# Optimization experiments

Measured on AMD Instinct MI355X. Metric: run time of the kernel, lower is better.

## Reference

```python
import jax, jax.numpy as jnp
import numpy as np

DIM_HEAD = 64
HEADS = 8

def rotate_half(x):
    x1, x2 = jnp.split(x, 2, axis=-1)
    return jnp.concatenate((-x2, x1), axis=-1)

def apply_rope(pos, t):
    # pos: [N, d] broadcast against t: [B, H, N, d]
    return t * jnp.cos(pos) + rotate_half(t) * jnp.sin(pos)

def setup_inputs() -> dict:
    key = jax.random.key(0)
    k1, k2, k3, k4 = jax.random.split(key, 4)
    B, N, C = 2, 4096, 512
    inner = HEADS * DIM_HEAD
    x = jax.random.normal(k1, (B, N, C), dtype=jnp.float32)
    pos_emb = jax.random.normal(k2, (N, DIM_HEAD), dtype=jnp.float32)
    w_qkv = jax.random.normal(k3, (C, inner * 3), dtype=jnp.float32) * (1.0 / np.sqrt(C))
    w_out = jax.random.normal(k4, (inner, C), dtype=jnp.float32) * (1.0 / np.sqrt(inner))
    b_out = jnp.zeros((C,), dtype=jnp.float32)
    return {"x": x, "pos_emb": pos_emb, "w_qkv": w_qkv, "w_out": w_out, "b_out": b_out}

def reference(x, pos_emb, w_qkv, w_out, b_out):
    B, N, C = x.shape
    scale = DIM_HEAD ** -0.5
    qkv = x @ w_qkv  # [B, N, 3*inner]
    q, k, v = jnp.split(qkv, 3, axis=-1)
    def to_heads(t):
        return t.reshape(B, N, HEADS, DIM_HEAD).transpose(0, 2, 1, 3)  # [B,H,N,d]
    q, k, v = to_heads(q), to_heads(k), to_heads(v)
    q = apply_rope(pos_emb, q)
    k = apply_rope(pos_emb, k)
    dots = jnp.einsum('bhid,bhjd->bhij', q, k) * scale  # [B,H,N,N]
    attn = jax.nn.softmax(dots, axis=-1)
    out = jnp.einsum('bhij,bhjd->bhid', attn, v)
    out = out.transpose(0, 2, 1, 3).reshape(B, N, HEADS * DIM_HEAD)
    return out @ w_out + b_out
```

## Files before the change

### kernel.cpp

```cpp
#include <hip/hip_runtime.h>


typedef float    floatx4 __attribute__((ext_vector_type(4)));
typedef _Float16 half8   __attribute__((ext_vector_type(8)));
typedef _Float16 half4   __attribute__((ext_vector_type(4)));

__device__ __forceinline__ float fast_exp2(float x) {
#if __has_builtin(__builtin_amdgcn_exp2f)
  return __builtin_amdgcn_exp2f(x);
#else
  float r;
  asm("v_exp_f32 %0, %1" : "=v"(r) : "v"(x));
  return r;
#endif
}

__device__ __forceinline__ void async16(const void* g, void* l) {
  __builtin_amdgcn_global_load_lds(
      (const __attribute__((address_space(1))) void*)g,
      (__attribute__((address_space(3))) void*)l, 16, 0, 0);
}

__global__ __launch_bounds__(256) void prep(
    const float* __restrict__ X, const float* __restrict__ pos,
    const float* __restrict__ Wqkv, const float* __restrict__ Wout,
    _Float16* __restrict__ A2, float2* __restrict__ CSSN,
    _Float16* __restrict__ B2qkv, _Float16* __restrict__ B2out) {
  __shared__ float tile[64][65];
  const int bid = blockIdx.x, t = threadIdx.x;
  if (bid < 4096) {
    const int i = (bid * 256 + t) * 4;
    const float4 v = *(const float4*)(X + i);
    half4 h;
    h[0] = (_Float16)v.x; h[1] = (_Float16)v.y;
    h[2] = (_Float16)v.z; h[3] = (_Float16)v.w;
    *(half4*)(A2 + i) = h;
  } else if (bid < 5120) {
    const int i = (bid - 4096) * 256 + t;
    const float p = pos[i];
    CSSN[i] = make_float2(__cosf(p), __sinf(p));
  } else {
    const float* W; _Float16* B2T; int Ncols, bx, by;
    if (bid < 5312) { const int idx = bid - 5120; bx = idx % 24; by = idx / 24;
                      W = Wqkv; B2T = B2qkv; Ncols = 1536; }
    else            { const int idx = bid - 5312; bx = idx % 8;  by = idx / 8;
                      W = Wout; B2T = B2out; Ncols = 512; }
    const int k0 = by * 64, n0 = bx * 64;
    const int lane = t & 63, w = t >> 6;
#pragma unroll 4
    for (int i = 0; i < 16; ++i) {
      const int k = w * 16 + i;
      tile[k][lane] = W[(size_t)(k0 + k) * Ncols + n0 + lane];
    }
    __syncthreads();
#pragma unroll 4
    for (int i = 0; i < 16; ++i) {
      const int n = w * 16 + i;
      B2T[(size_t)(n0 + n) * 512 + k0 + lane] = (_Float16)tile[lane][n];
    }
  }
}

__global__ __launch_bounds__(256) void gemm_qkv_rope(
    const _Float16* __restrict__ A2, const _Float16* __restrict__ B2T,
    const float2* __restrict__ CSSN,
    _Float16* __restrict__ Qb, _Float16* __restrict__ Kb,
    _Float16* __restrict__ VT) {
  __shared__ __align__(16) _Float16 ldsA[128 * 64];
  __shared__ __align__(16) _Float16 ldsB[128 * 64];
  __shared__ __align__(16) _Float16 qk_lds[4][16][72];
  const int t = threadIdx.x, w = t >> 6, l = t & 63;
  const int lo = l & 15, hi = l >> 4, sw = lo & 7;
  const int m0 = blockIdx.y << 7, n0 = blockIdx.x << 7;

  const int strow = w * 8 + (l >> 3);
  const int schunk = (l & 7) ^ ((l >> 3) & 7);
  const _Float16* gA = A2 + (size_t)(m0 + strow) * 512 + schunk * 8;
  const _Float16* gB = B2T + (size_t)(n0 + strow) * 512 + schunk * 8;
  _Float16* lA = ldsA + w * 512 + l * 8;
  _Float16* lB = ldsB + w * 512 + l * 8;

  const int mw = (w >> 1) * 64, nw = (w & 1) * 64;

  floatx4 acc[4][4];
#pragma unroll
  for (int mt = 0; mt < 4; ++mt)
#pragma unroll
    for (int nt = 0; nt < 4; ++nt) acc[mt][nt] = (floatx4){0.f, 0.f, 0.f, 0.f};

  for (int ks = 0; ks < 8; ++ks) {
    const int kk = ks * 64;
    __syncthreads();
#pragma unroll
    for (int i = 0; i < 4; ++i) {
      async16(gA + (size_t)i * 32 * 512 + kk, lA + i * 2048);
      async16(gB + (size_t)i * 32 * 512 + kk, lB + i * 2048);
    }
    __syncthreads();
#pragma unroll
    for (int kc = 0; kc < 2; ++kc) {
      const int slot = ((hi + 4 * kc) ^ sw) * 8;
      half8 af[4], bf[4];
#pragma unroll
      for (int mt = 0; mt < 4; ++mt)
        af[mt] = *(const half8*)(ldsA + (mw + mt * 16 + lo) * 64 + slot);
#pragma unroll
      for (int nt = 0; nt < 4; ++nt)
        bf[nt] = *(const half8*)(ldsB + (nw + nt * 16 + lo) * 64 + slot);
#pragma unroll
      for (int mt = 0; mt < 4; ++mt)
#pragma unroll
        for (int nt = 0; nt < 4; ++nt)
          acc[mt][nt] = __builtin_amdgcn_mfma_f32_16x16x32_f16(
              af[mt], bf[nt], acc[mt][nt], 0, 0, 0);
    }
  }

  const int bx = blockIdx.x;
  const int kind = bx >> 2;
  const int h = ((bx & 3) << 1) | (nw >> 6);
  if (kind == 2) {
#pragma unroll
    for (int mt = 0; mt < 4; ++mt) {
      const int rowb = m0 + mw + mt * 16 + hi * 4;
      const int b = rowb >> 12, nn = rowb & 4095;
#pragma unroll
      for (int nt = 0; nt < 4; ++nt) {
        const int dd = nt * 16 + lo;
        half4 v4;
#pragma unroll
        for (int r = 0; r < 4; ++r) v4[r] = (_Float16)acc[mt][nt][r];
        *(half4*)(VT + ((size_t)((b * 8 + h) * 64 + dd)) * 4096 + nn) = v4;
      }
    }
  } else {
    _Float16* Db = (kind == 0) ? Qb : Kb;
    const float sc = (kind == 0) ? 0.125f * 1.44269504f : 1.0f;
    _Float16 (*qt_)[72] = qk_lds[w];
#pragma unroll
    for (int mt = 0; mt < 4; ++mt) {
#pragma unroll
      for (int r = 0; r < 4; ++r) {
        const int row = m0 + mw + mt * 16 + hi * 4 + r;
        const int nn = row & 4095;
        const float2* cp = CSSN + (size_t)nn * 64 + lo;
#pragma unroll
        for (int nt = 0; nt < 4; ++nt) {
          const float2 cs = cp[nt * 16];
          const float x0 = acc[mt][nt][r];
          const float xp = acc[mt][nt ^ 2][r];
          const float rot = (nt & 2) ? xp : -xp;
          qt_[hi * 4 + r][nt * 16 + lo] = (_Float16)((x0 * cs.x + rot * cs.y) * sc);
        }
      }
#pragma unroll
      for (int pass = 0; pass < 2; ++pass) {
        const int rr = pass * 8 + (l >> 3);
        const int dcol = (l & 7) * 8;
        const half8 v = *(const half8*)&qt_[rr][dcol];
        const int row = m0 + mw + mt * 16 + rr;
        const int b = row >> 12, nn = row & 4095;
        *(half8*)(Db + ((size_t)((b * 8 + h) * 4096 + nn)) * 64 + dcol) = v;
      }
    }
  }
}

__global__ __launch_bounds__(256) void gemm_out_f16(
    const _Float16* __restrict__ A2, const _Float16* __restrict__ B2T,
    const float* __restrict__ bias, float* __restrict__ C) {
  __shared__ __align__(16) _Float16 ldsA[128 * 64];
  __shared__ __align__(16) _Float16 ldsB[64 * 64];
  const int t = threadIdx.x, w = t >> 6, l = t & 63;
  const int lo = l & 15, hi = l >> 4, sw = lo & 7;
  const int m0 = blockIdx.y << 7, n0 = blockIdx.x << 6;

  const int strow = w * 8 + (l >> 3);
  const int schunk = (l & 7) ^ ((l >> 3) & 7);
  const _Float16* gA = A2 + (size_t)(m0 + strow) * 512 + schunk * 8;
  const _Float16* gB = B2T + (size_t)(n0 + strow) * 512 + schunk * 8;
  _Float16* lA = ldsA + w * 512 + l * 8;
  _Float16* lB = ldsB + w * 512 + l * 8;

  const int mw = (w >> 1) * 64, nw = (w & 1) * 32;

  floatx4 acc[4][2];
#pragma unroll
  for (int mt = 0; mt < 4; ++mt)
#pragma unroll
    for (int nt = 0; nt < 2; ++nt) acc[mt][nt] = (floatx4){0.f, 0.f, 0.f, 0.f};

  for (int ks = 0; ks < 8; ++ks) {
    const int kk = ks * 64;
    __syncthreads();
#pragma unroll
    for (int i = 0; i < 4; ++i)
      async16(gA + (size_t)i * 32 * 512 + kk, lA + i * 2048);
#pragma unroll
    for (int i = 0; i < 2; ++i)
      async16(gB + (size_t)i * 32 * 512 + kk, lB + i * 2048);
    __syncthreads();
#pragma unroll
    for (int kc = 0; kc < 2; ++kc) {
      const int slot = ((hi + 4 * kc) ^ sw) * 8;
      half8 af[4], bf[2];
#pragma unroll
      for (int mt = 0; mt < 4; ++mt)
        af[mt] = *(const half8*)(ldsA + (mw + mt * 16 + lo) * 64 + slot);
#pragma unroll
      for (int nt = 0; nt < 2; ++nt)
        bf[nt] = *(const half8*)(ldsB + (nw + nt * 16 + lo) * 64 + slot);
#pragma unroll
      for (int mt = 0; mt < 4; ++mt)
#pragma unroll
        for (int nt = 0; nt < 2; ++nt)
          acc[mt][nt] = __builtin_amdgcn_mfma_f32_16x16x32_f16(
              af[mt], bf[nt], acc[mt][nt], 0, 0, 0);
    }
  }
#pragma unroll
  for (int mt = 0; mt < 4; ++mt)
#pragma unroll
    for (int r = 0; r < 4; ++r) {
      const int row = m0 + mw + mt * 16 + hi * 4 + r;
#pragma unroll
      for (int nt = 0; nt < 2; ++nt) {
        const int col = n0 + nw + nt * 16 + lo;
        C[(size_t)row * 512 + col] = acc[mt][nt][r] + bias[col];
      }
    }
}

__global__ __launch_bounds__(256, 4) void flash_attn(
    const _Float16* __restrict__ Qb, const _Float16* __restrict__ Kb,
    const _Float16* __restrict__ VT, _Float16* __restrict__ Opart,
    float* __restrict__ lpart) {
  __shared__ __align__(16) _Float16 ldsK[64 * 64];
  __shared__ __align__(16) _Float16 ldsV[64 * 64];
  const int t = threadIdx.x;
  const int w = t >> 6, l = t & 63;
  const int lo = l & 15, hi = l >> 4;
  const int sw = lo & 7;
  const int bh = blockIdx.y, qt = blockIdx.x, sp = blockIdx.z;

  const int srow = l >> 3;
  const int scol = (l & 7) ^ srow;
  const int goffK = srow * 64 + scol * 8;
  const size_t goffV = (size_t)srow * 4096 + scol * 8;
  const int ldst = l * 8;

  const _Float16* Qrow = Qb + ((size_t)bh * 4096 + qt * 128 + w * 32 + lo) * 64;
  half8 qf[2][2];
  qf[0][0] = *(const half8*)(Qrow + hi * 8);
  qf[0][1] = *(const half8*)(Qrow + hi * 8 + 32);
  qf[1][0] = *(const half8*)(Qrow + 16 * 64 + hi * 8);
  qf[1][1] = *(const half8*)(Qrow + 16 * 64 + hi * 8 + 32);

  floatx4 acc[2][4];
  float l_s[2] = {0.f, 0.f};
#pragma unroll
  for (int g = 0; g < 2; ++g)
#pragma unroll
    for (int dt = 0; dt < 4; ++dt) acc[g][dt] = (floatx4){0.f, 0.f, 0.f, 0.f};

  const _Float16* Kt = Kb + (size_t)bh * 4096 * 64;
  const _Float16* Vt = VT + (size_t)bh * 64 * 4096;

  for (int tt = sp * 32; tt < sp * 32 + 32; ++tt) {
    __syncthreads();
    {
      const _Float16* gK = Kt + (size_t)tt * 4096;
      const _Float16* gV = Vt + tt * 64;
      const int k0 = w * 2;
      async16(gK + (size_t)k0 * 512 + goffK,       ldsK + k0 * 512 + ldst);
      async16(gK + (size_t)(k0 + 1) * 512 + goffK, ldsK + (k0 + 1) * 512 + ldst);
      async16(gV + (size_t)k0 * 32768 + goffV,       ldsV + k0 * 512 + ldst);
      async16(gV + (size_t)(k0 + 1) * 32768 + goffV, ldsV + (k0 + 1) * 512 + ldst);
    }
    __syncthreads();

    floatx4 st[2][4];
#pragma unroll
    for (int jt = 0; jt < 4; ++jt) {
      const _Float16* kr = ldsK + (jt * 16 + lo) * 64;
      const half8 kf0 = *(const half8*)(kr + ((hi ^ sw) * 8));
      const half8 kf1 = *(const half8*)(kr + (((hi + 4) ^ sw) * 8));
#pragma unroll
      for (int g = 0; g < 2; ++g) {
        floatx4 z = (floatx4){0.f, 0.f, 0.f, 0.f};
        z = __builtin_amdgcn_mfma_f32_16x16x32_f16(kf0, qf[g][0], z, 0, 0, 0);
        z = __builtin_amdgcn_mfma_f32_16x16x32_f16(kf1, qf[g][1], z, 0, 0, 0);
        st[g][jt] = z;
      }
    }

    half4 pf[2][4];
#pragma unroll
    for (int g = 0; g < 2; ++g)
#pragma unroll
      for (int jt = 0; jt < 4; ++jt) {
        const float e0 = fast_exp2(st[g][jt][0]);
        const float e1 = fast_exp2(st[g][jt][1]);
        const float e2 = fast_exp2(st[g][jt][2]);
        const float e3 = fast_exp2(st[g][jt][3]);
        l_s[g] += (e0 + e1) + (e2 + e3);
        uint2 u;
        u.x = __builtin_bit_cast(unsigned, __builtin_amdgcn_cvt_pkrtz(e0, e1));
        u.y = __builtin_bit_cast(unsigned, __builtin_amdgcn_cvt_pkrtz(e2, e3));
        pf[g][jt] = __builtin_bit_cast(half4, u);
      }

#pragma unroll
    for (int dt = 0; dt < 4; ++dt) {
      half4 vf[4];
#pragma unroll
      for (int jt = 0; jt < 4; ++jt)
        vf[jt] = *(const half4*)(ldsV + (dt * 16 + lo) * 64 +
                                 (((jt * 2 + (hi >> 1)) ^ sw) * 8) + (hi & 1) * 4);
#pragma unroll
      for (int g = 0; g < 2; ++g)
#pragma unroll
        for (int jt = 0; jt < 4; ++jt)
          acc[g][dt] = __builtin_amdgcn_mfma_f32_16x16x16f16(
              pf[g][jt], vf[jt], acc[g][dt], 0, 0, 0);
    }
  }

  _Float16* obase = Opart + ((size_t)(sp * 16 + bh)) * 4096 * 64;
  float*    lbase = lpart + ((size_t)(sp * 16 + bh)) * 4096;
#pragma unroll
  for (int g = 0; g < 2; ++g) {
    float v = l_s[g];
    v += __shfl_xor(v, 16);
    v += __shfl_xor(v, 32);
    if (hi == 0)
      lbase[qt * 128 + w * 32 + g * 16 + lo] = v;
#pragma unroll
    for (int r = 0; r < 4; ++r) {
      const int q = qt * 128 + w * 32 + g * 16 + hi * 4 + r;
#pragma unroll
      for (int dt = 0; dt < 4; ++dt)
        obase[(size_t)q * 64 + dt * 16 + lo] = (_Float16)acc[g][dt][r];
    }
  }
}

__global__ __launch_bounds__(256) void combine_splits(
    const _Float16* __restrict__ Opart, const float* __restrict__ lpart,
    _Float16* __restrict__ O2) {
  const int idx = blockIdx.x * 256 + threadIdx.x;
  const int d0 = (idx & 15) * 4;
  const int q  = (idx >> 4) & 4095;
  const int bh = idx >> 16;
  const int b = bh >> 3, h = bh & 7;
  const half4 a0 = *(const half4*)(Opart + ((size_t)bh * 4096 + q) * 64 + d0);
  const half4 a1 = *(const half4*)(Opart + ((size_t)(16 + bh) * 4096 + q) * 64 + d0);
  const float lsum = lpart[(size_t)bh * 4096 + q] +
                     lpart[(size_t)(16 + bh) * 4096 + q];
  const float inv = 1.f / lsum;
  half4 o;
#pragma unroll
  for (int i = 0; i < 4; ++i)
    o[i] = (_Float16)(((float)a0[i] + (float)a1[i]) * inv);
  *(half4*)(O2 + ((size_t)(b * 4096 + q)) * 512 + h * 64 + d0) = o;
}

extern "C" void kernel_launch(void* const* d_in, const int* in_sizes, int n_in,
                              void* d_out, int out_size, void* d_ws, size_t ws_size,
                              hipStream_t stream) {
  const float* x     = (const float*)d_in[0];
  const float* pos   = (const float*)d_in[1];
  const float* w_qkv = (const float*)d_in[2];
  const float* w_out = (const float*)d_in[3];
  const float* b_out = (const float*)d_in[4];
  float* out = (float*)d_out;

  char* ws = (char*)d_ws;
  if (ws_size < (size_t)56 * 1024 * 1024) return;

  const size_t MB = 1024 * 1024;
  _Float16* A2x   = (_Float16*)ws;
  _Float16* O2    = (_Float16*)ws;
  _Float16* B2qkv = (_Float16*)(ws + 8 * MB);
  float2*   CSSN  = (float2*)(ws + 11 * MB);
  _Float16* Qb    = (_Float16*)(ws + 13 * MB);
  _Float16* Kb    = (_Float16*)(ws + 21 * MB);
  _Float16* VT    = (_Float16*)(ws + 29 * MB);
  _Float16* Opart = (_Float16*)(ws + 37 * MB);
  float*    lpart = (float*)(ws + 53 * MB);
  _Float16* B2out = (_Float16*)(ws + 54 * MB);

  prep<<<5376, 256, 0, stream>>>(x, pos, w_qkv, w_out, A2x, CSSN, B2qkv, B2out);
  gemm_qkv_rope<<<dim3(12, 64), 256, 0, stream>>>(A2x, B2qkv, CSSN, Qb, Kb, VT);
  flash_attn<<<dim3(32, 16, 2), 256, 0, stream>>>(Qb, Kb, VT, Opart, lpart);
  combine_splits<<<4096, 256, 0, stream>>>(Opart, lpart, O2);
  gemm_out_f16<<<dim3(8, 64), 256, 0, stream>>>(O2, B2out, b_out, out);
}
```

Before: 206.3 us.

## Fuse split-combine into output GEMM and narrow QKV GEMM tiles

Drops the separate combine_splits kernel. The output projection GEMM now reads both flash-attention partial outputs and their row sums directly, normalizes them, and stores the result into LDS as its A operand, one head per K step. This saves a launch and a round trip of the combined O through global memory. The cost is that these A loads become synchronous register loads instead of async LDS loads. The QKV GEMM also changes from 128x128 to 128x64 tiles, doubling the grid and reusing ldsA as the RoPE staging buffer to cut LDS use, which lowers reuse per block.

```diff
diff --git a/kernel.cpp b/kernel.cpp
--- a/kernel.cpp
+++ b/kernel.cpp
@@ -67,11 +67,10 @@
     _Float16* __restrict__ Qb, _Float16* __restrict__ Kb,
     _Float16* __restrict__ VT) {
   __shared__ __align__(16) _Float16 ldsA[128 * 64];
-  __shared__ __align__(16) _Float16 ldsB[128 * 64];
-  __shared__ __align__(16) _Float16 qk_lds[4][16][72];
+  __shared__ __align__(16) _Float16 ldsB[64 * 64];
   const int t = threadIdx.x, w = t >> 6, l = t & 63;
   const int lo = l & 15, hi = l >> 4, sw = lo & 7;
-  const int m0 = blockIdx.y << 7, n0 = blockIdx.x << 7;
+  const int m0 = blockIdx.y << 7, n0 = blockIdx.x << 6;
 
   const int strow = w * 8 + (l >> 3);
   const int schunk = (l & 7) ^ ((l >> 3) & 7);
@@ -80,11 +79,11 @@
   _Float16* lA = ldsA + w * 512 + l * 8;
   _Float16* lB = ldsB + w * 512 + l * 8;
 
-  const int mw = (w >> 1) * 64, nw = (w & 1) * 64;
-
-  floatx4 acc[4][4];
-#pragma unroll
-  for (int mt = 0; mt < 4; ++mt)
+  const int mw = w * 32;
+
+  floatx4 acc[2][4];
+#pragma unroll
+  for (int mt = 0; mt < 2; ++mt)
 #pragma unroll
     for (int nt = 0; nt < 4; ++nt) acc[mt][nt] = (floatx4){0.f, 0.f, 0.f, 0.f};
 
@@ -92,23 +91,24 @@
     const int kk = ks * 64;
     __syncthreads();
 #pragma unroll
-    for (int i = 0; i < 4; ++i) {
+    for (int i = 0; i < 4; ++i)
       async16(gA + (size_t)i * 32 * 512 + kk, lA + i * 2048);
+#pragma unroll
+    for (int i = 0; i < 2; ++i)
       async16(gB + (size_t)i * 32 * 512 + kk, lB + i * 2048);
-    }
     __syncthreads();
 #pragma unroll
     for (int kc = 0; kc < 2; ++kc) {
       const int slot = ((hi + 4 * kc) ^ sw) * 8;
-      half8 af[4], bf[4];
-#pragma unroll
-      for (int mt = 0; mt < 4; ++mt)
+      half8 af[2], bf[4];
+#pragma unroll
+      for (int mt = 0; mt < 2; ++mt)
         af[mt] = *(const half8*)(ldsA + (mw + mt * 16 + lo) * 64 + slot);
 #pragma unroll
       for (int nt = 0; nt < 4; ++nt)
-        bf[nt] = *(const half8*)(ldsB + (nw + nt * 16 + lo) * 64 + slot);
-#pragma unroll
-      for (int mt = 0; mt < 4; ++mt)
+        bf[nt] = *(const half8*)(ldsB + (nt * 16 + lo) * 64 + slot);
+#pragma unroll
+      for (int mt = 0; mt < 2; ++mt)
 #pragma unroll
         for (int nt = 0; nt < 4; ++nt)
           acc[mt][nt] = __builtin_amdgcn_mfma_f32_16x16x32_f16(
@@ -117,11 +117,11 @@
   }
 
   const int bx = blockIdx.x;
-  const int kind = bx >> 2;
-  const int h = ((bx & 3) << 1) | (nw >> 6);
+  const int kind = bx >> 3;
+  const int h = bx & 7;
   if (kind == 2) {
 #pragma unroll
-    for (int mt = 0; mt < 4; ++mt) {
+    for (int mt = 0; mt < 2; ++mt) {
       const int rowb = m0 + mw + mt * 16 + hi * 4;
       const int b = rowb >> 12, nn = rowb & 4095;
 #pragma unroll
@@ -134,11 +134,12 @@
       }
     }
   } else {
-    _Float16* Db = (kind == 0) ? Qb : Kb;
+    _Float16* Db = kind ? Kb : Qb;
     const float sc = (kind == 0) ? 0.125f * 1.44269504f : 1.0f;
-    _Float16 (*qt_)[72] = qk_lds[w];
-#pragma unroll
-    for (int mt = 0; mt < 4; ++mt) {
+    __syncthreads();
+    _Float16 (*qt_)[72] = (_Float16(*)[72])(ldsA + w * 2048);
+#pragma unroll
+    for (int mt = 0; mt < 2; ++mt) {
 #pragma unroll
       for (int r = 0; r < 4; ++r) {
         const int row = m0 + mw + mt * 16 + hi * 4 + r;
@@ -167,17 +168,23 @@
 }
 
 __global__ __launch_bounds__(256) void gemm_out_f16(
-    const _Float16* __restrict__ A2, const _Float16* __restrict__ B2T,
-    const float* __restrict__ bias, float* __restrict__ C) {
+    const _Float16* __restrict__ Opart, const float* __restrict__ lpart,
+    const _Float16* __restrict__ B2T, const float* __restrict__ bias,
+    float* __restrict__ C) {
   __shared__ __align__(16) _Float16 ldsA[128 * 64];
   __shared__ __align__(16) _Float16 ldsB[64 * 64];
   const int t = threadIdx.x, w = t >> 6, l = t & 63;
   const int lo = l & 15, hi = l >> 4, sw = lo & 7;
   const int m0 = blockIdx.y << 7, n0 = blockIdx.x << 6;
+  const int b = m0 >> 12, q0 = m0 & 4095;
 
   const int strow = w * 8 + (l >> 3);
   const int schunk = (l & 7) ^ ((l >> 3) & 7);
-  const _Float16* gA = A2 + (size_t)(m0 + strow) * 512 + schunk * 8;
+  const size_t aRow = (size_t)(q0 + strow) * 64 + schunk * 8;
+  const _Float16* gA0 = Opart + ((size_t)(b * 8)) * 4096 * 64 + aRow;
+  const _Float16* gA1 = Opart + ((size_t)(16 + b * 8)) * 4096 * 64 + aRow;
+  const float* lp0 = lpart + (size_t)(b * 8) * 4096 + q0 + strow;
+  const float* lp1 = lpart + (size_t)(16 + b * 8) * 4096 + q0 + strow;
   const _Float16* gB = B2T + (size_t)(n0 + strow) * 512 + schunk * 8;
   _Float16* lA = ldsA + w * 512 + l * 8;
   _Float16* lB = ldsB + w * 512 + l * 8;
@@ -192,10 +199,20 @@
 
   for (int ks = 0; ks < 8; ++ks) {
     const int kk = ks * 64;
-    __syncthreads();
-#pragma unroll
-    for (int i = 0; i < 4; ++i)
-      async16(gA + (size_t)i * 32 * 512 + kk, lA + i * 2048);
+    const size_t hoff = (size_t)ks * 4096 * 64;
+    const int lhoff = ks * 4096;
+    __syncthreads();
+#pragma unroll
+    for (int i = 0; i < 4; ++i) {
+      const half8 o0 = *(const half8*)(gA0 + hoff + (size_t)i * 32 * 64);
+      const half8 o1 = *(const half8*)(gA1 + hoff + (size_t)i * 32 * 64);
+      const float ls = lp0[lhoff + i * 32] + lp1[lhoff + i * 32];
+      const _Float16 inv = (_Float16)(1.f / ls);
+      half8 s;
+#pragma unroll
+      for (int j = 0; j < 8; ++j) s[j] = (_Float16)((o0[j] + o1[j]) * inv);
+      *(half8*)(lA + i * 2048) = s;
+    }
 #pragma unroll
     for (int i = 0; i < 2; ++i)
       async16(gB + (size_t)i * 32 * 512 + kk, lB + i * 2048);
@@ -345,26 +362,6 @@
   }
 }
 
-__global__ __launch_bounds__(256) void combine_splits(
-    const _Float16* __restrict__ Opart, const float* __restrict__ lpart,
-    _Float16* __restrict__ O2) {
-  const int idx = blockIdx.x * 256 + threadIdx.x;
-  const int d0 = (idx & 15) * 4;
-  const int q  = (idx >> 4) & 4095;
-  const int bh = idx >> 16;
-  const int b = bh >> 3, h = bh & 7;
-  const half4 a0 = *(const half4*)(Opart + ((size_t)bh * 4096 + q) * 64 + d0);
-  const half4 a1 = *(const half4*)(Opart + ((size_t)(16 + bh) * 4096 + q) * 64 + d0);
-  const float lsum = lpart[(size_t)bh * 4096 + q] +
-                     lpart[(size_t)(16 + bh) * 4096 + q];
-  const float inv = 1.f / lsum;
-  half4 o;
-#pragma unroll
-  for (int i = 0; i < 4; ++i)
-    o[i] = (_Float16)(((float)a0[i] + (float)a1[i]) * inv);
-  *(half4*)(O2 + ((size_t)(b * 4096 + q)) * 512 + h * 64 + d0) = o;
-}
-
 extern "C" void kernel_launch(void* const* d_in, const int* in_sizes, int n_in,
                               void* d_out, int out_size, void* d_ws, size_t ws_size,
                               hipStream_t stream) {
@@ -380,7 +377,6 @@
 
   const size_t MB = 1024 * 1024;
   _Float16* A2x   = (_Float16*)ws;
-  _Float16* O2    = (_Float16*)ws;
   _Float16* B2qkv = (_Float16*)(ws + 8 * MB);
   float2*   CSSN  = (float2*)(ws + 11 * MB);
   _Float16* Qb    = (_Float16*)(ws + 13 * MB);
@@ -391,8 +387,7 @@
   _Float16* B2out = (_Float16*)(ws + 54 * MB);
 
   prep<<<5376, 256, 0, stream>>>(x, pos, w_qkv, w_out, A2x, CSSN, B2qkv, B2out);
-  gemm_qkv_rope<<<dim3(12, 64), 256, 0, stream>>>(A2x, B2qkv, CSSN, Qb, Kb, VT);
+  gemm_qkv_rope<<<dim3(24, 64), 256, 0, stream>>>(A2x, B2qkv, CSSN, Qb, Kb, VT);
   flash_attn<<<dim3(32, 16, 2), 256, 0, stream>>>(Qb, Kb, VT, Opart, lpart);
-  combine_splits<<<4096, 256, 0, stream>>>(Opart, lpart, O2);
-  gemm_out_f16<<<dim3(8, 64), 256, 0, stream>>>(O2, B2out, b_out, out);
-}
+  gemm_out_f16<<<dim3(8, 64), 256, 0, stream>>>(Opart, lpart, B2out, b_out, out);
+}
```

Result: slower. 216.9 us (+5.1%).
